# Kernel tuning notes

Measured on AMD Instinct MI355X. Metric: run time of the kernel, lower is better.

The kernel has to match this reference:

```python
import jax, jax.numpy as jnp
import numpy as np
from jax import lax

B, S, I, H, L = 128, 256, 64, 128, 64
N_SUB = 2  # fixed RK4 substeps per observation interval (replaces adaptive dopri5)


def setup_inputs() -> dict:
    key = jax.random.key(0)
    ks = jax.random.split(key, 16)
    sc = 0.05
    x = jax.random.normal(ks[0], (B, S, I), jnp.float32)
    # strictly increasing irregular observation times
    times = jnp.sort(jax.random.uniform(ks[1], (S,), jnp.float32) * 10.0)
    return {
        "x": x,
        "times": times,
        "W_ih": jax.random.normal(ks[2], (3 * H, I), jnp.float32) * sc,
        "W_hh": jax.random.normal(ks[3], (3 * H, H), jnp.float32) * sc,
        "b_ih": jnp.zeros((3 * H,), jnp.float32),
        "b_hh": jnp.zeros((3 * H,), jnp.float32),
        "ode_W1": jax.random.normal(ks[4], (H, H), jnp.float32) * sc,
        "ode_b1": jnp.zeros((H,), jnp.float32),
        "ode_W2": jax.random.normal(ks[5], (H, H), jnp.float32) * sc,
        "ode_b2": jnp.zeros((H,), jnp.float32),
        "W_mean": jax.random.normal(ks[6], (L, H), jnp.float32) * sc,
        "b_mean": jnp.zeros((L,), jnp.float32),
        "W_logvar": jax.random.normal(ks[7], (L, H), jnp.float32) * sc,
        "b_logvar": jnp.zeros((L,), jnp.float32),
    }


def reference(x, times, W_ih, W_hh, b_ih, b_hh, ode_W1, ode_b1, ode_W2, ode_b2,
              W_mean, b_mean, W_logvar, b_logvar):
    def ode_f(h):  # MLP dynamics: Linear -> tanh -> Linear (time-independent)
        return jnp.tanh(h @ ode_W1.T + ode_b1) @ ode_W2.T + ode_b2

    def rk4(h, dt):
        k1 = ode_f(h)
        k2 = ode_f(h + 0.5 * dt * k1)
        k3 = ode_f(h + 0.5 * dt * k2)
        k4 = ode_f(h + dt * k3)
        return h + (dt / 6.0) * (k1 + 2.0 * k2 + 2.0 * k3 + k4)

    def gru(x_t, h):  # torch.nn.GRUCell math
        gx = x_t @ W_ih.T + b_ih
        gh = h @ W_hh.T + b_hh
        rx, zx, nx = jnp.split(gx, 3, axis=-1)
        rh, zh, nh = jnp.split(gh, 3, axis=-1)
        r = jax.nn.sigmoid(rx + rh)
        z = jax.nn.sigmoid(zx + zh)
        n = jnp.tanh(nx + r * nh)
        return (1.0 - z) * n + z * h

    # iterate i = S-1 .. 0; before each GRU update (except the first, i=S-1)
    # evolve h from t_{i+1} backward to t_i  -> dt_i = t_i - t_{i+1} (negative)
    dt_rev = jnp.concatenate([jnp.zeros((1,), times.dtype),
                              (times[:-1] - times[1:])[::-1]])  # [S]
    x_rev = jnp.transpose(x[:, ::-1, :], (1, 0, 2))  # [S, B, I]

    def step(h, inp):
        x_t, dt = inp
        sub = dt / N_SUB
        for _ in range(N_SUB):  # fixed small unroll
            h = rk4(h, sub)
        h = gru(x_t, h)
        return h, None

    h0 = jnp.zeros((x.shape[0], W_hh.shape[1]), x.dtype)
    h, _ = lax.scan(step, h0, (x_rev, dt_rev))
    mean = h @ W_mean.T + b_mean
    logvar = h @ W_logvar.T + b_logvar
    return (mean, logvar)
```

## Files before the change

### kernel.cpp

```cpp
#include <hip/hip_runtime.h>

#define NB 128
#define NS 256
#define NI 64
#define NH 128
#define NL 64
#define NG 384

typedef _Float16 f16;
typedef __attribute__((ext_vector_type(2))) _Float16 f16x2;

__device__ __forceinline__ float fast_tanh(float x) {
    float e = __expf(2.0f * x);
    return 1.0f - 2.0f / (e + 1.0f);
}
__device__ __forceinline__ float fast_sig(float x) {
    return 1.0f / (1.0f + __expf(-x));
}
__device__ __forceinline__ float quad_red(float a) {
    a += __shfl_xor(a, 1);
    a += __shfl_xor(a, 2);
    return a;
}
__device__ __forceinline__ float fdot2(f16x2 a, f16x2 b, float c) {
#if __has_builtin(__builtin_amdgcn_fdot2)
    return __builtin_amdgcn_fdot2(a, b, c, false);
#else
    return c + (float)a.x * (float)b.x + (float)a.y * (float)b.y;
#endif
}
__device__ __forceinline__ f16x2 bc16(unsigned int u) {
    return __builtin_bit_cast(f16x2, u);
}

__device__ __align__(16) f16 g_W1h[NH * NH];
__device__ __align__(16) f16 g_W2h[NH * NH];
__device__ __align__(16) f16 g_W12h[NH * NH];
__device__ __align__(16) f16 g_Whhh[3 * NH * NH];
__device__ __align__(16) f16 g_Whh2h[3 * NH * NH];
__device__ float g_w1b2[NH];
__device__ float g_whhb2[3 * NH];

__global__ __launch_bounds__(384)
void gx_kernel(const float* __restrict__ x, const float* __restrict__ W_ih,
               const float* __restrict__ b_ih, float* __restrict__ gx)
{
    const int s = blockIdx.x;
    const int j = threadIdx.x;
    __shared__ __align__(16) float xs[NB * NI];
    for (int idx = j; idx < NB * NI; idx += 384) {
        int bb = idx >> 6, cc = idx & 63;
        xs[idx] = x[(bb * NS + s) * NI + cc];
    }
    float w[64];
#pragma unroll
    for (int c = 0; c < 64; c += 4)
        *(float4*)&w[c] = *(const float4*)&W_ih[j * NI + c];
    const float bj = b_ih[j];
    __syncthreads();
    for (int bb = 0; bb < NB; bb++) {
        const float* xr = xs + bb * NI;
        float a0 = 0.f, a1 = 0.f, a2 = 0.f, a3 = 0.f;
#pragma unroll
        for (int c = 0; c < 64; c += 4) {
            a0 = fmaf(w[c + 0], xr[c + 0], a0);
            a1 = fmaf(w[c + 1], xr[c + 1], a1);
            a2 = fmaf(w[c + 2], xr[c + 2], a2);
            a3 = fmaf(w[c + 3], xr[c + 3], a3);
        }
        gx[((size_t)s * NB + bb) * NG + j] = ((a0 + a1) + (a2 + a3)) + bj;
    }
}

__global__ __launch_bounds__(128)
void prep_kernel(const float* __restrict__ W1, const float* __restrict__ Whh,
                 const float* __restrict__ W2, const float* __restrict__ b2)
{
    const int i = blockIdx.x;
    const int j = threadIdx.x;
    __shared__ float rowA[NH];
    __shared__ float red[NH];
    const float* src = (i < NH) ? (W1 + i * NH) : (Whh + (size_t)(i - NH) * NH);
    rowA[j] = src[j];
    __syncthreads();
    float acc = 0.f;
    for (int k = 0; k < NH; k++) acc = fmaf(rowA[k], W2[k * NH + j], acc);
    if (i < NH) {
        g_W12h[i * NH + j] = (f16)acc;
        g_W1h[i * NH + j]  = (f16)rowA[j];
        g_W2h[i * NH + j]  = (f16)W2[i * NH + j];
    } else {
        g_Whh2h[(size_t)(i - NH) * NH + j] = (f16)acc;
        g_Whhh[(size_t)(i - NH) * NH + j]  = (f16)rowA[j];
    }
    red[j] = rowA[j] * b2[j];
    __syncthreads();
    for (int off = 64; off > 0; off >>= 1) {
        if (j < off) red[j] += red[j + off];
        __syncthreads();
    }
    if (j == 0) {
        if (i < NH) g_w1b2[i] = red[0];
        else        g_whhb2[i - NH] = red[0];
    }
}

#define CH(SRC, OBX) (*(const uint4*)((const unsigned char*)(SRC) + (OBX)))

#define DSTEP1(W, K, V, A0, A1)                                                \
    A0 = fdot2(W[K + 0], bc16((V).x), A0);                                     \
    A1 = fdot2(W[K + 1], bc16((V).y), A1);                                     \
    A0 = fdot2(W[K + 2], bc16((V).z), A0);                                     \
    A1 = fdot2(W[K + 3], bc16((V).w), A1);

#define DOT1(W, SRC, OUT)                                                      \
    {                                                                          \
        float a0_ = 0.f, a1_ = 0.f;                                            \
        { uint4 v_ = CH(SRC, ob0); DSTEP1(W, 0,  v_, a0_, a1_) }               \
        { uint4 v_ = CH(SRC, ob1); DSTEP1(W, 4,  v_, a0_, a1_) }               \
        { uint4 v_ = CH(SRC, ob2); DSTEP1(W, 8,  v_, a0_, a1_) }               \
        { uint4 v_ = CH(SRC, ob3); DSTEP1(W, 12, v_, a0_, a1_) }               \
        OUT = quad_red(a0_ + a1_);                                             \
    }

#define DOT2S(WA, WB, SRC, OA, OB)                                             \
    {                                                                          \
        float a0_ = 0.f, a1_ = 0.f, b0_ = 0.f, b1_ = 0.f;                      \
        { uint4 v_ = CH(SRC, ob0); DSTEP1(WA, 0,  v_, a0_, a1_) DSTEP1(WB, 0,  v_, b0_, b1_) } \
        { uint4 v_ = CH(SRC, ob1); DSTEP1(WA, 4,  v_, a0_, a1_) DSTEP1(WB, 4,  v_, b0_, b1_) } \
        { uint4 v_ = CH(SRC, ob2); DSTEP1(WA, 8,  v_, a0_, a1_) DSTEP1(WB, 8,  v_, b0_, b1_) } \
        { uint4 v_ = CH(SRC, ob3); DSTEP1(WA, 12, v_, a0_, a1_) DSTEP1(WB, 12, v_, b0_, b1_) } \
        OA = quad_red(a0_ + a1_);                                              \
        OB = quad_red(b0_ + b1_);                                              \
    }

#define DOT2D(WA, SA, WB, SB, OA, OB)                                          \
    {                                                                          \
        float a0_ = 0.f, a1_ = 0.f, b0_ = 0.f, b1_ = 0.f;                      \
        { uint4 v_ = CH(SA, ob0); uint4 u_ = CH(SB, ob0); DSTEP1(WA, 0,  v_, a0_, a1_) DSTEP1(WB, 0,  u_, b0_, b1_) } \
        { uint4 v_ = CH(SA, ob1); uint4 u_ = CH(SB, ob1); DSTEP1(WA, 4,  v_, a0_, a1_) DSTEP1(WB, 4,  u_, b0_, b1_) } \
        { uint4 v_ = CH(SA, ob2); uint4 u_ = CH(SB, ob2); DSTEP1(WA, 8,  v_, a0_, a1_) DSTEP1(WB, 8,  u_, b0_, b1_) } \
        { uint4 v_ = CH(SA, ob3); uint4 u_ = CH(SB, ob3); DSTEP1(WA, 12, v_, a0_, a1_) DSTEP1(WB, 12, u_, b0_, b1_) } \
        OA = quad_red(a0_ + a1_);                                              \
        OB = quad_red(b0_ + b1_);                                              \
    }

#define DOT4S(WA, WB, WC, WD, SRC, OA, OB, OC, OD)                             \
    {                                                                          \
        float a0_ = 0.f, a1_ = 0.f, b0_ = 0.f, b1_ = 0.f;                      \
        float c0_ = 0.f, c1_ = 0.f, d0_ = 0.f, d1_ = 0.f;                      \
        { uint4 v_ = CH(SRC, ob0); DSTEP1(WA, 0,  v_, a0_, a1_) DSTEP1(WB, 0,  v_, b0_, b1_) DSTEP1(WC, 0,  v_, c0_, c1_) DSTEP1(WD, 0,  v_, d0_, d1_) } \
        { uint4 v_ = CH(SRC, ob1); DSTEP1(WA, 4,  v_, a0_, a1_) DSTEP1(WB, 4,  v_, b0_, b1_) DSTEP1(WC, 4,  v_, c0_, c1_) DSTEP1(WD, 4,  v_, d0_, d1_) } \
        { uint4 v_ = CH(SRC, ob2); DSTEP1(WA, 8,  v_, a0_, a1_) DSTEP1(WB, 8,  v_, b0_, b1_) DSTEP1(WC, 8,  v_, c0_, c1_) DSTEP1(WD, 8,  v_, d0_, d1_) } \
        { uint4 v_ = CH(SRC, ob3); DSTEP1(WA, 12, v_, a0_, a1_) DSTEP1(WB, 12, v_, b0_, b1_) DSTEP1(WC, 12, v_, c0_, c1_) DSTEP1(WD, 12, v_, d0_, d1_) } \
        OA = quad_red(a0_ + a1_);                                              \
        OB = quad_red(b0_ + b1_);                                              \
        OC = quad_red(c0_ + c1_);                                              \
        OD = quad_red(d0_ + d1_);                                              \
    }

#define LOADW(DST, BASE)                                                       \
    {                                                                          \
        uint4 v0_ = *(const uint4*)((BASE) + cb0);                             \
        DST[0] = bc16(v0_.x); DST[1] = bc16(v0_.y); DST[2] = bc16(v0_.z); DST[3] = bc16(v0_.w); \
        uint4 v1_ = *(const uint4*)((BASE) + cb1);                             \
        DST[4] = bc16(v1_.x); DST[5] = bc16(v1_.y); DST[6] = bc16(v1_.z); DST[7] = bc16(v1_.w); \
        uint4 v2_ = *(const uint4*)((BASE) + cb2);                             \
        DST[8] = bc16(v2_.x); DST[9] = bc16(v2_.y); DST[10] = bc16(v2_.z); DST[11] = bc16(v2_.w); \
        uint4 v3_ = *(const uint4*)((BASE) + cb3);                             \
        DST[12] = bc16(v3_.x); DST[13] = bc16(v3_.y); DST[14] = bc16(v3_.z); DST[15] = bc16(v3_.w); \
    }

__global__ __launch_bounds__(512, 1)
void rnn_kernel(const float* __restrict__ times, const float* __restrict__ b_hh,
                const float* __restrict__ b1, const float* __restrict__ b2,
                const float* __restrict__ W_mean, const float* __restrict__ b_mean,
                const float* __restrict__ W_logvar, const float* __restrict__ b_logvar,
                const float* __restrict__ gx,
                const float* __restrict__ x, const float* __restrict__ W_ih,
                const float* __restrict__ b_ih,
                const int use_gx,
                float* __restrict__ out)
{
    const int b = blockIdx.x;
    const int t = threadIdx.x;
    const int r = t >> 2;
    const int p = t & 3;
    const int c0 = 32 * p;

    __shared__ __align__(16) f16 shHh[NH], shUh[NH], shAh[NH];
    __shared__ float shT[NS];
    __shared__ __align__(16) float shGX[NG], shX[NI], shHf[NH];

    const int cb0 = c0 + 8 * ((0 + p) & 3);
    const int cb1 = c0 + 8 * ((1 + p) & 3);
    const int cb2 = c0 + 8 * ((2 + p) & 3);
    const int cb3 = c0 + 8 * ((3 + p) & 3);
    const int ob0 = 2 * cb0, ob1 = 2 * cb1, ob2 = 2 * cb2, ob3 = 2 * cb3;

    f16x2 w1p[16], w2p[16], w12p[16];
    f16x2 wh0p[16], wh1p[16], wh2p[16];
    f16x2 ws0p[16], ws1p[16], ws2p[16];
    LOADW(w1p,  g_W1h  + r * NH);
    LOADW(w2p,  g_W2h  + r * NH);
    LOADW(w12p, g_W12h + r * NH);
    LOADW(wh0p, g_Whhh + (0 * NH + r) * NH);
    LOADW(wh1p, g_Whhh + (1 * NH + r) * NH);
    LOADW(wh2p, g_Whhh + (2 * NH + r) * NH);
    LOADW(ws0p, g_Whh2h + (size_t)(0 * NH + r) * NH);
    LOADW(ws1p, g_Whh2h + (size_t)(1 * NH + r) * NH);
    LOADW(ws2p, g_Whh2h + (size_t)(2 * NH + r) * NH);

    const float b1r = b1[r], b2r = b2[r];
    const float bh0 = b_hh[r], bh1 = b_hh[NH + r], bh2 = b_hh[2 * NH + r];
    const float w1b2r = g_w1b2[r];
    const float wb0 = g_whhb2[r], wb1 = g_whhb2[NH + r], wb2 = g_whhb2[2 * NH + r];

    if (t < NS) shT[t] = times[t];
    if (t < NH) shHh[t] = (f16)0.f;
    float h = 0.f;
    __syncthreads();

    for (int si = 0; si < NS; ++si) {
        const int seq = NS - 1 - si;
        const float dt = (si == 0) ? 0.f : (shT[seq] - shT[seq + 1]);
        const float dts = 0.5f * dt;
        const float a2 = 0.5f * dts;
        const float a6 = dts * (1.f / 6.f);

        float gxr = 0.f, gxz = 0.f, gxn = 0.f;
        if (use_gx) {
            const float* g = gx + ((size_t)seq * NB + b) * NG;
            gxr = g[r]; gxz = g[NH + r]; gxn = g[2 * NH + r];
        } else {
            if (t < NI) shX[t] = x[(b * NS + seq) * NI + t];
            __syncthreads();
            if (t < NG) {
                const float* wr = W_ih + t * NI;
                float a = 0.f;
#pragma unroll
                for (int cc = 0; cc < NI; cc += 4) {
                    float4 w4 = *(const float4*)(wr + cc);
                    a = fmaf(w4.x, shX[cc + 0], a);
                    a = fmaf(w4.y, shX[cc + 1], a);
                    a = fmaf(w4.z, shX[cc + 2], a);
                    a = fmaf(w4.w, shX[cc + 3], a);
                }
                shGX[t] = a + b_ih[t];
            }
            __syncthreads();
        }

        float z1a, u, S, m;
        DOT1(w1p, shHh, z1a);
        z1a += b1r;
        u = fast_tanh(z1a);
        S = u;
        if (p == 0) shUh[r] = (f16)u;
        __syncthreads();
        DOT1(w12p, shUh, m);
        u = fast_tanh(z1a + a2 * (m + w1b2r));
        S += 2.f * u;
        if (p == 0) shUh[r] = (f16)u;
        __syncthreads();
        DOT1(w12p, shUh, m);
        u = fast_tanh(z1a + a2 * (m + w1b2r));
        S += 2.f * u;
        if (p == 0) shUh[r] = (f16)u;
        __syncthreads();
        DOT1(w12p, shUh, m);
        u = fast_tanh(z1a + dts * (m + w1b2r));
        S += u;
        if (p == 0) shUh[r] = (f16)S;
        __syncthreads();
        float mA, mB;
        DOT2S(w2p, w12p, shUh, mA, mB);
        const float hA = h + a6 * mA + dts * b2r;
        const float z1b = z1a + a6 * mB + dts * w1b2r;
        u = fast_tanh(z1b);
        float S2 = u;
        if (p == 0) { shAh[r] = (f16)hA; shUh[r] = (f16)u; }
        __syncthreads();

        float g0, g1, g2;
        DOT2D(w12p, shUh, wh0p, shAh, m, g0);
        u = fast_tanh(z1b + a2 * (m + w1b2r));
        S2 += 2.f * u;
        if (p == 0) shUh[r] = (f16)u;
        __syncthreads();
        DOT2D(w12p, shUh, wh1p, shAh, m, g1);
        u = fast_tanh(z1b + a2 * (m + w1b2r));
        S2 += 2.f * u;
        if (p == 0) shUh[r] = (f16)u;
        __syncthreads();
        DOT2D(w12p, shUh, wh2p, shAh, m, g2);
        u = fast_tanh(z1b + dts * (m + w1b2r));
        S2 += u;
        if (p == 0) shUh[r] = (f16)S2;
        __syncthreads();
        float n0, n1, n2, n3;
        DOT4S(w2p, ws0p, ws1p, ws2p, shUh, n0, n1, n2, n3);
        const float hB = hA + a6 * n0 + dts * b2r;
        const float rh = g0 + a6 * n1 + dts * wb0 + bh0;
        const float zh = g1 + a6 * n2 + dts * wb1 + bh1;
        const float nh = g2 + a6 * n3 + dts * wb2 + bh2;
        float rx, zx, nx;
        if (use_gx) { rx = gxr; zx = gxz; nx = gxn; }
        else        { rx = shGX[r]; zx = shGX[NH + r]; nx = shGX[2 * NH + r]; }
        const float rr = fast_sig(rx + rh);
        const float zz = fast_sig(zx + zh);
        const float nn = fast_tanh(nx + rr * nh);
        h = (1.f - zz) * nn + zz * hB;
        if (p == 0) shHh[r] = (f16)h;
        __syncthreads();
    }

    if (p == 0) shHf[r] = h;
    __syncthreads();
    const int sel = r >> 6;
    const int l = r & 63;
    const float* Wf = sel ? W_logvar : W_mean;
    float a0 = 0.f, a1 = 0.f;
#pragma unroll
    for (int jj = 0; jj < 8; jj++) {
        float4 w4 = *(const float4*)&Wf[l * NH + c0 + 4 * jj];
        float4 h4 = *(const float4*)(shHf + c0 + 4 * jj);
        a0 = fmaf(w4.x, h4.x, a0);
        a1 = fmaf(w4.y, h4.y, a1);
        a0 = fmaf(w4.z, h4.z, a0);
        a1 = fmaf(w4.w, h4.w, a1);
    }
    float acc = quad_red(a0 + a1);
    if (p == 0) {
        const float bias = sel ? b_logvar[l] : b_mean[l];
        out[sel * (NB * NL) + b * NL + l] = acc + bias;
    }
}

extern "C" void kernel_launch(void* const* d_in, const int* in_sizes, int n_in,
                              void* d_out, int out_size, void* d_ws, size_t ws_size,
                              hipStream_t stream)
{
    const float* x        = (const float*)d_in[0];
    const float* times    = (const float*)d_in[1];
    const float* W_ih     = (const float*)d_in[2];
    const float* W_hh     = (const float*)d_in[3];
    const float* b_ih     = (const float*)d_in[4];
    const float* b_hh     = (const float*)d_in[5];
    const float* W1       = (const float*)d_in[6];
    const float* b1       = (const float*)d_in[7];
    const float* W2       = (const float*)d_in[8];
    const float* b2       = (const float*)d_in[9];
    const float* W_mean   = (const float*)d_in[10];
    const float* b_mean   = (const float*)d_in[11];
    const float* W_logvar = (const float*)d_in[12];
    const float* b_logvar = (const float*)d_in[13];
    float* out = (float*)d_out;

    float* gxbuf = (float*)d_ws;
    const size_t need = (size_t)NS * NB * NG * sizeof(float);
    const int use_gx = (d_ws != nullptr && ws_size >= need) ? 1 : 0;

    if (use_gx) {
        gx_kernel<<<NS, 384, 0, stream>>>(x, W_ih, b_ih, gxbuf);
    }
    prep_kernel<<<512, 128, 0, stream>>>(W1, W_hh, W2, b2);
    rnn_kernel<<<NB, 512, 0, stream>>>(times, b_hh, b1, b2,
                                       W_mean, b_mean, W_logvar, b_logvar,
                                       gxbuf, x, W_ih, b_ih, use_gx, out);
}
```

Baseline: 967.4 us.

## Halve threads per row to two lanes and prefetch next step's gx

The recurrent kernel now uses 256 threads per batch element, each hidden row split across 2 lanes of 64 columns instead of 4 lanes of 32. Each lane keeps twice as many fp16 weight registers and needs only one shuffle in its reduction instead of two. The input-gate values for the next timestep are loaded one iteration early so their global-memory latency overlaps the current step. In exchange, register pressure roughly doubles (9×32 packed weight registers per thread), and each lane's serial dot product is longer.

```diff
diff --git a/kernel.cpp b/kernel.cpp
--- a/kernel.cpp
+++ b/kernel.cpp
@@ -17,9 +17,8 @@
 __device__ __forceinline__ float fast_sig(float x) {
     return 1.0f / (1.0f + __expf(-x));
 }
-__device__ __forceinline__ float quad_red(float a) {
+__device__ __forceinline__ float red2(float a) {
     a += __shfl_xor(a, 1);
-    a += __shfl_xor(a, 2);
     return a;
 }
 __device__ __forceinline__ float fdot2(f16x2 a, f16x2 b, float c) {
@@ -105,9 +104,9 @@
     }
 }
 
-#define CH(SRC, OBX) (*(const uint4*)((const unsigned char*)(SRC) + (OBX)))
-
-#define DSTEP1(W, K, V, A0, A1)                                                \
+#define CHNK(SRC, OB) (*(const uint4*)((const unsigned char*)(SRC) + (OB)))
+
+#define D4(W, K, V, A0, A1)                                                    \
     A0 = fdot2(W[K + 0], bc16((V).x), A0);                                     \
     A1 = fdot2(W[K + 1], bc16((V).y), A1);                                     \
     A0 = fdot2(W[K + 2], bc16((V).z), A0);                                     \
@@ -116,62 +115,82 @@
 #define DOT1(W, SRC, OUT)                                                      \
     {                                                                          \
         float a0_ = 0.f, a1_ = 0.f;                                            \
-        { uint4 v_ = CH(SRC, ob0); DSTEP1(W, 0,  v_, a0_, a1_) }               \
-        { uint4 v_ = CH(SRC, ob1); DSTEP1(W, 4,  v_, a0_, a1_) }               \
-        { uint4 v_ = CH(SRC, ob2); DSTEP1(W, 8,  v_, a0_, a1_) }               \
-        { uint4 v_ = CH(SRC, ob3); DSTEP1(W, 12, v_, a0_, a1_) }               \
-        OUT = quad_red(a0_ + a1_);                                             \
+        { uint4 v_ = CHNK(SRC, ob0); D4(W, 0,  v_, a0_, a1_) }                 \
+        { uint4 v_ = CHNK(SRC, ob1); D4(W, 4,  v_, a0_, a1_) }                 \
+        { uint4 v_ = CHNK(SRC, ob2); D4(W, 8,  v_, a0_, a1_) }                 \
+        { uint4 v_ = CHNK(SRC, ob3); D4(W, 12, v_, a0_, a1_) }                 \
+        { uint4 v_ = CHNK(SRC, ob4); D4(W, 16, v_, a0_, a1_) }                 \
+        { uint4 v_ = CHNK(SRC, ob5); D4(W, 20, v_, a0_, a1_) }                 \
+        { uint4 v_ = CHNK(SRC, ob6); D4(W, 24, v_, a0_, a1_) }                 \
+        { uint4 v_ = CHNK(SRC, ob7); D4(W, 28, v_, a0_, a1_) }                 \
+        OUT = red2(a0_ + a1_);                                                 \
     }
 
 #define DOT2S(WA, WB, SRC, OA, OB)                                             \
     {                                                                          \
         float a0_ = 0.f, a1_ = 0.f, b0_ = 0.f, b1_ = 0.f;                      \
-        { uint4 v_ = CH(SRC, ob0); DSTEP1(WA, 0,  v_, a0_, a1_) DSTEP1(WB, 0,  v_, b0_, b1_) } \
-        { uint4 v_ = CH(SRC, ob1); DSTEP1(WA, 4,  v_, a0_, a1_) DSTEP1(WB, 4,  v_, b0_, b1_) } \
-        { uint4 v_ = CH(SRC, ob2); DSTEP1(WA, 8,  v_, a0_, a1_) DSTEP1(WB, 8,  v_, b0_, b1_) } \
-        { uint4 v_ = CH(SRC, ob3); DSTEP1(WA, 12, v_, a0_, a1_) DSTEP1(WB, 12, v_, b0_, b1_) } \
-        OA = quad_red(a0_ + a1_);                                              \
-        OB = quad_red(b0_ + b1_);                                              \
+        { uint4 v_ = CHNK(SRC, ob0); D4(WA, 0,  v_, a0_, a1_) D4(WB, 0,  v_, b0_, b1_) } \
+        { uint4 v_ = CHNK(SRC, ob1); D4(WA, 4,  v_, a0_, a1_) D4(WB, 4,  v_, b0_, b1_) } \
+        { uint4 v_ = CHNK(SRC, ob2); D4(WA, 8,  v_, a0_, a1_) D4(WB, 8,  v_, b0_, b1_) } \
+        { uint4 v_ = CHNK(SRC, ob3); D4(WA, 12, v_, a0_, a1_) D4(WB, 12, v_, b0_, b1_) } \
+        { uint4 v_ = CHNK(SRC, ob4); D4(WA, 16, v_, a0_, a1_) D4(WB, 16, v_, b0_, b1_) } \
+        { uint4 v_ = CHNK(SRC, ob5); D4(WA, 20, v_, a0_, a1_) D4(WB, 20, v_, b0_, b1_) } \
+        { uint4 v_ = CHNK(SRC, ob6); D4(WA, 24, v_, a0_, a1_) D4(WB, 24, v_, b0_, b1_) } \
+        { uint4 v_ = CHNK(SRC, ob7); D4(WA, 28, v_, a0_, a1_) D4(WB, 28, v_, b0_, b1_) } \
+        OA = red2(a0_ + a1_);                                                  \
+        OB = red2(b0_ + b1_);                                                  \
     }
 
 #define DOT2D(WA, SA, WB, SB, OA, OB)                                          \
     {                                                                          \
         float a0_ = 0.f, a1_ = 0.f, b0_ = 0.f, b1_ = 0.f;                      \
-        { uint4 v_ = CH(SA, ob0); uint4 u_ = CH(SB, ob0); DSTEP1(WA, 0,  v_, a0_, a1_) DSTEP1(WB, 0,  u_, b0_, b1_) } \
-        { uint4 v_ = CH(SA, ob1); uint4 u_ = CH(SB, ob1); DSTEP1(WA, 4,  v_, a0_, a1_) DSTEP1(WB, 4,  u_, b0_, b1_) } \
-        { uint4 v_ = CH(SA, ob2); uint4 u_ = CH(SB, ob2); DSTEP1(WA, 8,  v_, a0_, a1_) DSTEP1(WB, 8,  u_, b0_, b1_) } \
-        { uint4 v_ = CH(SA, ob3); uint4 u_ = CH(SB, ob3); DSTEP1(WA, 12, v_, a0_, a1_) DSTEP1(WB, 12, u_, b0_, b1_) } \
-        OA = quad_red(a0_ + a1_);                                              \
-        OB = quad_red(b0_ + b1_);                                              \
+        { uint4 v_ = CHNK(SA, ob0); uint4 u_ = CHNK(SB, ob0); D4(WA, 0,  v_, a0_, a1_) D4(WB, 0,  u_, b0_, b1_) } \
+        { uint4 v_ = CHNK(SA, ob1); uint4 u_ = CHNK(SB, ob1); D4(WA, 4,  v_, a0_, a1_) D4(WB, 4,  u_, b0_, b1_) } \
+        { uint4 v_ = CHNK(SA, ob2); uint4 u_ = CHNK(SB, ob2); D4(WA, 8,  v_, a0_, a1_) D4(WB, 8,  u_, b0_, b1_) } \
+        { uint4 v_ = CHNK(SA, ob3); uint4 u_ = CHNK(SB, ob3); D4(WA, 12, v_, a0_, a1_) D4(WB, 12, u_, b0_, b1_) } \
+        { uint4 v_ = CHNK(SA, ob4); uint4 u_ = CHNK(SB, ob4); D4(WA, 16, v_, a0_, a1_) D4(WB, 16, u_, b0_, b1_) } \
+        { uint4 v_ = CHNK(SA, ob5); uint4 u_ = CHNK(SB, ob5); D4(WA, 20, v_, a0_, a1_) D4(WB, 20, u_, b0_, b1_) } \
+        { uint4 v_ = CHNK(SA, ob6); uint4 u_ = CHNK(SB, ob6); D4(WA, 24, v_, a0_, a1_) D4(WB, 24, u_, b0_, b1_) } \
+        { uint4 v_ = CHNK(SA, ob7); uint4 u_ = CHNK(SB, ob7); D4(WA, 28, v_, a0_, a1_) D4(WB, 28, u_, b0_, b1_) } \
+        OA = red2(a0_ + a1_);                                                  \
+        OB = red2(b0_ + b1_);                                                  \
     }
 
 #define DOT4S(WA, WB, WC, WD, SRC, OA, OB, OC, OD)                             \
     {                                                                          \
         float a0_ = 0.f, a1_ = 0.f, b0_ = 0.f, b1_ = 0.f;                      \
         float c0_ = 0.f, c1_ = 0.f, d0_ = 0.f, d1_ = 0.f;                      \
-        { uint4 v_ = CH(SRC, ob0); DSTEP1(WA, 0,  v_, a0_, a1_) DSTEP1(WB, 0,  v_, b0_, b1_) DSTEP1(WC, 0,  v_, c0_, c1_) DSTEP1(WD, 0,  v_, d0_, d1_) } \
-        { uint4 v_ = CH(SRC, ob1); DSTEP1(WA, 4,  v_, a0_, a1_) DSTEP1(WB, 4,  v_, b0_, b1_) DSTEP1(WC, 4,  v_, c0_, c1_) DSTEP1(WD, 4,  v_, d0_, d1_) } \
-        { uint4 v_ = CH(SRC, ob2); DSTEP1(WA, 8,  v_, a0_, a1_) DSTEP1(WB, 8,  v_, b0_, b1_) DSTEP1(WC, 8,  v_, c0_, c1_) DSTEP1(WD, 8,  v_, d0_, d1_) } \
-        { uint4 v_ = CH(SRC, ob3); DSTEP1(WA, 12, v_, a0_, a1_) DSTEP1(WB, 12, v_, b0_, b1_) DSTEP1(WC, 12, v_, c0_, c1_) DSTEP1(WD, 12, v_, d0_, d1_) } \
-        OA = quad_red(a0_ + a1_);                                              \
-        OB = quad_red(b0_ + b1_);                                              \
-        OC = quad_red(c0_ + c1_);                                              \
-        OD = quad_red(d0_ + d1_);                                              \
+        { uint4 v_ = CHNK(SRC, ob0); D4(WA, 0,  v_, a0_, a1_) D4(WB, 0,  v_, b0_, b1_) D4(WC, 0,  v_, c0_, c1_) D4(WD, 0,  v_, d0_, d1_) } \
+        { uint4 v_ = CHNK(SRC, ob1); D4(WA, 4,  v_, a0_, a1_) D4(WB, 4,  v_, b0_, b1_) D4(WC, 4,  v_, c0_, c1_) D4(WD, 4,  v_, d0_, d1_) } \
+        { uint4 v_ = CHNK(SRC, ob2); D4(WA, 8,  v_, a0_, a1_) D4(WB, 8,  v_, b0_, b1_) D4(WC, 8,  v_, c0_, c1_) D4(WD, 8,  v_, d0_, d1_) } \
+        { uint4 v_ = CHNK(SRC, ob3); D4(WA, 12, v_, a0_, a1_) D4(WB, 12, v_, b0_, b1_) D4(WC, 12, v_, c0_, c1_) D4(WD, 12, v_, d0_, d1_) } \
+        { uint4 v_ = CHNK(SRC, ob4); D4(WA, 16, v_, a0_, a1_) D4(WB, 16, v_, b0_, b1_) D4(WC, 16, v_, c0_, c1_) D4(WD, 16, v_, d0_, d1_) } \
+        { uint4 v_ = CHNK(SRC, ob5); D4(WA, 20, v_, a0_, a1_) D4(WB, 20, v_, b0_, b1_) D4(WC, 20, v_, c0_, c1_) D4(WD, 20, v_, d0_, d1_) } \
+        { uint4 v_ = CHNK(SRC, ob6); D4(WA, 24, v_, a0_, a1_) D4(WB, 24, v_, b0_, b1_) D4(WC, 24, v_, c0_, c1_) D4(WD, 24, v_, d0_, d1_) } \
+        { uint4 v_ = CHNK(SRC, ob7); D4(WA, 28, v_, a0_, a1_) D4(WB, 28, v_, b0_, b1_) D4(WC, 28, v_, c0_, c1_) D4(WD, 28, v_, d0_, d1_) } \
+        OA = red2(a0_ + a1_);                                                  \
+        OB = red2(b0_ + b1_);                                                  \
+        OC = red2(c0_ + c1_);                                                  \
+        OD = red2(d0_ + d1_);                                                  \
+    }
+
+#define LDCH(DST, K, BP, OB)                                                   \
+    {                                                                          \
+        uint4 v_ = *(const uint4*)((BP) + (OB));                               \
+        DST[K + 0] = bc16(v_.x); DST[K + 1] = bc16(v_.y);                      \
+        DST[K + 2] = bc16(v_.z); DST[K + 3] = bc16(v_.w);                      \
     }
 
 #define LOADW(DST, BASE)                                                       \
     {                                                                          \
-        uint4 v0_ = *(const uint4*)((BASE) + cb0);                             \
-        DST[0] = bc16(v0_.x); DST[1] = bc16(v0_.y); DST[2] = bc16(v0_.z); DST[3] = bc16(v0_.w); \
-        uint4 v1_ = *(const uint4*)((BASE) + cb1);                             \
-        DST[4] = bc16(v1_.x); DST[5] = bc16(v1_.y); DST[6] = bc16(v1_.z); DST[7] = bc16(v1_.w); \
-        uint4 v2_ = *(const uint4*)((BASE) + cb2);                             \
-        DST[8] = bc16(v2_.x); DST[9] = bc16(v2_.y); DST[10] = bc16(v2_.z); DST[11] = bc16(v2_.w); \
-        uint4 v3_ = *(const uint4*)((BASE) + cb3);                             \
-        DST[12] = bc16(v3_.x); DST[13] = bc16(v3_.y); DST[14] = bc16(v3_.z); DST[15] = bc16(v3_.w); \
-    }
-
-__global__ __launch_bounds__(512, 1)
+        const unsigned char* bp_ = (const unsigned char*)(BASE);               \
+        LDCH(DST, 0,  bp_, ob0) LDCH(DST, 4,  bp_, ob1)                        \
+        LDCH(DST, 8,  bp_, ob2) LDCH(DST, 12, bp_, ob3)                        \
+        LDCH(DST, 16, bp_, ob4) LDCH(DST, 20, bp_, ob5)                        \
+        LDCH(DST, 24, bp_, ob6) LDCH(DST, 28, bp_, ob7)                        \
+    }
+
+__global__ __launch_bounds__(256, 1)
 void rnn_kernel(const float* __restrict__ times, const float* __restrict__ b_hh,
                 const float* __restrict__ b1, const float* __restrict__ b2,
                 const float* __restrict__ W_mean, const float* __restrict__ b_mean,
@@ -184,23 +203,25 @@
 {
     const int b = blockIdx.x;
     const int t = threadIdx.x;
-    const int r = t >> 2;
-    const int p = t & 3;
-    const int c0 = 32 * p;
+    const int r = t >> 1;
+    const int p = t & 1;
 
     __shared__ __align__(16) f16 shHh[NH], shUh[NH], shAh[NH];
     __shared__ float shT[NS];
     __shared__ __align__(16) float shGX[NG], shX[NI], shHf[NH];
 
-    const int cb0 = c0 + 8 * ((0 + p) & 3);
-    const int cb1 = c0 + 8 * ((1 + p) & 3);
-    const int cb2 = c0 + 8 * ((2 + p) & 3);
-    const int cb3 = c0 + 8 * ((3 + p) & 3);
-    const int ob0 = 2 * cb0, ob1 = 2 * cb1, ob2 = 2 * cb2, ob3 = 2 * cb3;
-
-    f16x2 w1p[16], w2p[16], w12p[16];
-    f16x2 wh0p[16], wh1p[16], wh2p[16];
-    f16x2 ws0p[16], ws1p[16], ws2p[16];
+    const int ob0 = 128 * p + 16 * ((0 + 4 * p) & 7);
+    const int ob1 = 128 * p + 16 * ((1 + 4 * p) & 7);
+    const int ob2 = 128 * p + 16 * ((2 + 4 * p) & 7);
+    const int ob3 = 128 * p + 16 * ((3 + 4 * p) & 7);
+    const int ob4 = 128 * p + 16 * ((4 + 4 * p) & 7);
+    const int ob5 = 128 * p + 16 * ((5 + 4 * p) & 7);
+    const int ob6 = 128 * p + 16 * ((6 + 4 * p) & 7);
+    const int ob7 = 128 * p + 16 * ((7 + 4 * p) & 7);
+
+    f16x2 w1p[32], w2p[32], w12p[32];
+    f16x2 wh0p[32], wh1p[32], wh2p[32];
+    f16x2 ws0p[32], ws1p[32], ws2p[32];
     LOADW(w1p,  g_W1h  + r * NH);
     LOADW(w2p,  g_W2h  + r * NH);
     LOADW(w12p, g_W12h + r * NH);
@@ -221,6 +242,12 @@
     float h = 0.f;
     __syncthreads();
 
+    float gxr = 0.f, gxz = 0.f, gxn = 0.f;
+    if (use_gx) {
+        const float* g = gx + ((size_t)(NS - 1) * NB + b) * NG;
+        gxr = g[r]; gxz = g[NH + r]; gxn = g[2 * NH + r];
+    }
+
     for (int si = 0; si < NS; ++si) {
         const int seq = NS - 1 - si;
         const float dt = (si == 0) ? 0.f : (shT[seq] - shT[seq + 1]);
@@ -228,15 +255,16 @@
         const float a2 = 0.5f * dts;
         const float a6 = dts * (1.f / 6.f);
 
-        float gxr = 0.f, gxz = 0.f, gxn = 0.f;
+        float gnr = 0.f, gnz = 0.f, gnn = 0.f;
         if (use_gx) {
-            const float* g = gx + ((size_t)seq * NB + b) * NG;
-            gxr = g[r]; gxz = g[NH + r]; gxn = g[2 * NH + r];
+            const int seqn = (seq > 0) ? (seq - 1) : 0;
+            const float* g = gx + ((size_t)seqn * NB + b) * NG;
+            gnr = g[r]; gnz = g[NH + r]; gnn = g[2 * NH + r];
         } else {
             if (t < NI) shX[t] = x[(b * NS + seq) * NI + t];
             __syncthreads();
-            if (t < NG) {
-                const float* wr = W_ih + t * NI;
+            for (int idx = t; idx < NG; idx += 256) {
+                const float* wr = W_ih + idx * NI;
                 float a = 0.f;
 #pragma unroll
                 for (int cc = 0; cc < NI; cc += 4) {
@@ -246,7 +274,7 @@
                     a = fmaf(w4.z, shX[cc + 2], a);
                     a = fmaf(w4.w, shX[cc + 3], a);
                 }
-                shGX[t] = a + b_ih[t];
+                shGX[idx] = a + b_ih[idx];
             }
             __syncthreads();
         }
@@ -312,6 +340,7 @@
         const float nn = fast_tanh(nx + rr * nh);
         h = (1.f - zz) * nn + zz * hB;
         if (p == 0) shHh[r] = (f16)h;
+        gxr = gnr; gxz = gnz; gxn = gnn;
         __syncthreads();
     }
 
@@ -320,17 +349,18 @@
     const int sel = r >> 6;
     const int l = r & 63;
     const float* Wf = sel ? W_logvar : W_mean;
+    const int hc0 = 64 * p;
     float a0 = 0.f, a1 = 0.f;
 #pragma unroll
-    for (int jj = 0; jj < 8; jj++) {
-        float4 w4 = *(const float4*)&Wf[l * NH + c0 + 4 * jj];
-        float4 h4 = *(const float4*)(shHf + c0 + 4 * jj);
+    for (int jj = 0; jj < 16; jj++) {
+        float4 w4 = *(const float4*)&Wf[l * NH + hc0 + 4 * jj];
+        float4 h4 = *(const float4*)(shHf + hc0 + 4 * jj);
         a0 = fmaf(w4.x, h4.x, a0);
         a1 = fmaf(w4.y, h4.y, a1);
         a0 = fmaf(w4.z, h4.z, a0);
         a1 = fmaf(w4.w, h4.w, a1);
     }
-    float acc = quad_red(a0 + a1);
+    float acc = red2(a0 + a1);
     if (p == 0) {
         const float bias = sel ? b_logvar[l] : b_mean[l];
         out[sel * (NB * NL) + b * NL + l] = acc + bias;
@@ -365,7 +395,7 @@
         gx_kernel<<<NS, 384, 0, stream>>>(x, W_ih, b_ih, gxbuf);
     }
     prep_kernel<<<512, 128, 0, stream>>>(W1, W_hh, W2, b2);
-    rnn_kernel<<<NB, 512, 0, stream>>>(times, b_hh, b1, b2,
+    rnn_kernel<<<NB, 256, 0, stream>>>(times, b_hh, b1, b2,
                                        W_mean, b_mean, W_logvar, b_logvar,
                                        gxbuf, x, W_ih, b_ih, use_gx, out);
 }
```

After: 1.061 ms. 9.7% more time.

## Use DPP quad reductions, lighter LDS barriers, and prefetch next-step gate inputs

Applied to the files above, without the earlier changes.

Replaces the shfl_xor quad reductions with DPP row-permute adds and the full __syncthreads with an LDS-only waitcnt plus s_barrier, to cut latency on the serial recurrence's critical path. It also prefetches the next timestep's precomputed input-gate values one iteration ahead, adds more independent dot-product accumulators in the small dot macros for ILP, and changes the launch bounds to allow two blocks per CU. The risks are register pressure from launch_bounds(512,2) causing weight-register spills, and subtle ordering hazards from the custom barrier.

```diff
diff --git a/kernel.cpp b/kernel.cpp
--- a/kernel.cpp
+++ b/kernel.cpp
@@ -17,9 +17,15 @@
 __device__ __forceinline__ float fast_sig(float x) {
     return 1.0f / (1.0f + __expf(-x));
 }
+template <int CTRL>
+__device__ __forceinline__ float dpp_xor_add(float a) {
+    int ai = __builtin_bit_cast(int, a);
+    int bi = __builtin_amdgcn_update_dpp(0, ai, CTRL, 0xF, 0xF, true);
+    return a + __builtin_bit_cast(float, bi);
+}
 __device__ __forceinline__ float quad_red(float a) {
-    a += __shfl_xor(a, 1);
-    a += __shfl_xor(a, 2);
+    a = dpp_xor_add<0xB1>(a);
+    a = dpp_xor_add<0x4E>(a);
     return a;
 }
 __device__ __forceinline__ float fdot2(f16x2 a, f16x2 b, float c) {
@@ -31,6 +37,11 @@
 }
 __device__ __forceinline__ f16x2 bc16(unsigned int u) {
     return __builtin_bit_cast(f16x2, u);
+}
+__device__ __forceinline__ void sync_lds() {
+    asm volatile("s_waitcnt lgkmcnt(0)" ::: "memory");
+    __builtin_amdgcn_s_barrier();
+    asm volatile("" ::: "memory");
 }
 
 __device__ __align__(16) f16 g_W1h[NH * NH];
@@ -105,9 +116,15 @@
     }
 }
 
-#define CH(SRC, OBX) (*(const uint4*)((const unsigned char*)(SRC) + (OBX)))
-
-#define DSTEP1(W, K, V, A0, A1)                                                \
+#define CHNK(SRC, OB) (*(const uint4*)((const unsigned char*)(SRC) + (OB)))
+
+#define D4(W, K, V, A0, A1, A2, A3)                                            \
+    A0 = fdot2(W[K + 0], bc16((V).x), A0);                                     \
+    A1 = fdot2(W[K + 1], bc16((V).y), A1);                                     \
+    A2 = fdot2(W[K + 2], bc16((V).z), A2);                                     \
+    A3 = fdot2(W[K + 3], bc16((V).w), A3);
+
+#define D2(W, K, V, A0, A1)                                                    \
     A0 = fdot2(W[K + 0], bc16((V).x), A0);                                     \
     A1 = fdot2(W[K + 1], bc16((V).y), A1);                                     \
     A0 = fdot2(W[K + 2], bc16((V).z), A0);                                     \
@@ -115,63 +132,67 @@
 
 #define DOT1(W, SRC, OUT)                                                      \
     {                                                                          \
-        float a0_ = 0.f, a1_ = 0.f;                                            \
-        { uint4 v_ = CH(SRC, ob0); DSTEP1(W, 0,  v_, a0_, a1_) }               \
-        { uint4 v_ = CH(SRC, ob1); DSTEP1(W, 4,  v_, a0_, a1_) }               \
-        { uint4 v_ = CH(SRC, ob2); DSTEP1(W, 8,  v_, a0_, a1_) }               \
-        { uint4 v_ = CH(SRC, ob3); DSTEP1(W, 12, v_, a0_, a1_) }               \
-        OUT = quad_red(a0_ + a1_);                                             \
+        float a0_ = 0.f, a1_ = 0.f, a2_ = 0.f, a3_ = 0.f;                      \
+        { uint4 v_ = CHNK(SRC, ob0); D4(W, 0,  v_, a0_, a1_, a2_, a3_) }       \
+        { uint4 v_ = CHNK(SRC, ob1); D4(W, 4,  v_, a0_, a1_, a2_, a3_) }       \
+        { uint4 v_ = CHNK(SRC, ob2); D4(W, 8,  v_, a0_, a1_, a2_, a3_) }       \
+        { uint4 v_ = CHNK(SRC, ob3); D4(W, 12, v_, a0_, a1_, a2_, a3_) }       \
+        OUT = quad_red((a0_ + a1_) + (a2_ + a3_));                             \
     }
 
 #define DOT2S(WA, WB, SRC, OA, OB)                                             \
     {                                                                          \
-        float a0_ = 0.f, a1_ = 0.f, b0_ = 0.f, b1_ = 0.f;                      \
-        { uint4 v_ = CH(SRC, ob0); DSTEP1(WA, 0,  v_, a0_, a1_) DSTEP1(WB, 0,  v_, b0_, b1_) } \
-        { uint4 v_ = CH(SRC, ob1); DSTEP1(WA, 4,  v_, a0_, a1_) DSTEP1(WB, 4,  v_, b0_, b1_) } \
-        { uint4 v_ = CH(SRC, ob2); DSTEP1(WA, 8,  v_, a0_, a1_) DSTEP1(WB, 8,  v_, b0_, b1_) } \
-        { uint4 v_ = CH(SRC, ob3); DSTEP1(WA, 12, v_, a0_, a1_) DSTEP1(WB, 12, v_, b0_, b1_) } \
-        OA = quad_red(a0_ + a1_);                                              \
-        OB = quad_red(b0_ + b1_);                                              \
+        float a0_ = 0.f, a1_ = 0.f, a2_ = 0.f, a3_ = 0.f;                      \
+        float b0_ = 0.f, b1_ = 0.f, b2_ = 0.f, b3_ = 0.f;                      \
+        { uint4 v_ = CHNK(SRC, ob0); D4(WA, 0,  v_, a0_, a1_, a2_, a3_) D4(WB, 0,  v_, b0_, b1_, b2_, b3_) } \
+        { uint4 v_ = CHNK(SRC, ob1); D4(WA, 4,  v_, a0_, a1_, a2_, a3_) D4(WB, 4,  v_, b0_, b1_, b2_, b3_) } \
+        { uint4 v_ = CHNK(SRC, ob2); D4(WA, 8,  v_, a0_, a1_, a2_, a3_) D4(WB, 8,  v_, b0_, b1_, b2_, b3_) } \
+        { uint4 v_ = CHNK(SRC, ob3); D4(WA, 12, v_, a0_, a1_, a2_, a3_) D4(WB, 12, v_, b0_, b1_, b2_, b3_) } \
+        OA = quad_red((a0_ + a1_) + (a2_ + a3_));                              \
+        OB = quad_red((b0_ + b1_) + (b2_ + b3_));                              \
     }
 
 #define DOT2D(WA, SA, WB, SB, OA, OB)                                          \
     {                                                                          \
-        float a0_ = 0.f, a1_ = 0.f, b0_ = 0.f, b1_ = 0.f;                      \
-        { uint4 v_ = CH(SA, ob0); uint4 u_ = CH(SB, ob0); DSTEP1(WA, 0,  v_, a0_, a1_) DSTEP1(WB, 0,  u_, b0_, b1_) } \
-        { uint4 v_ = CH(SA, ob1); uint4 u_ = CH(SB, ob1); DSTEP1(WA, 4,  v_, a0_, a1_) DSTEP1(WB, 4,  u_, b0_, b1_) } \
-        { uint4 v_ = CH(SA, ob2); uint4 u_ = CH(SB, ob2); DSTEP1(WA, 8,  v_, a0_, a1_) DSTEP1(WB, 8,  u_, b0_, b1_) } \
-        { uint4 v_ = CH(SA, ob3); uint4 u_ = CH(SB, ob3); DSTEP1(WA, 12, v_, a0_, a1_) DSTEP1(WB, 12, u_, b0_, b1_) } \
-        OA = quad_red(a0_ + a1_);                                              \
-        OB = quad_red(b0_ + b1_);                                              \
+        float a0_ = 0.f, a1_ = 0.f, a2_ = 0.f, a3_ = 0.f;                      \
+        float b0_ = 0.f, b1_ = 0.f, b2_ = 0.f, b3_ = 0.f;                      \
+        { uint4 v_ = CHNK(SA, ob0); uint4 u_ = CHNK(SB, ob0); D4(WA, 0,  v_, a0_, a1_, a2_, a3_) D4(WB, 0,  u_, b0_, b1_, b2_, b3_) } \
+        { uint4 v_ = CHNK(SA, ob1); uint4 u_ = CHNK(SB, ob1); D4(WA, 4,  v_, a0_, a1_, a2_, a3_) D4(WB, 4,  u_, b0_, b1_, b2_, b3_) } \
+        { uint4 v_ = CHNK(SA, ob2); uint4 u_ = CHNK(SB, ob2); D4(WA, 8,  v_, a0_, a1_, a2_, a3_) D4(WB, 8,  u_, b0_, b1_, b2_, b3_) } \
+        { uint4 v_ = CHNK(SA, ob3); uint4 u_ = CHNK(SB, ob3); D4(WA, 12, v_, a0_, a1_, a2_, a3_) D4(WB, 12, u_, b0_, b1_, b2_, b3_) } \
+        OA = quad_red((a0_ + a1_) + (a2_ + a3_));                              \
+        OB = quad_red((b0_ + b1_) + (b2_ + b3_));                              \
     }
 
 #define DOT4S(WA, WB, WC, WD, SRC, OA, OB, OC, OD)                             \
     {                                                                          \
         float a0_ = 0.f, a1_ = 0.f, b0_ = 0.f, b1_ = 0.f;                      \
         float c0_ = 0.f, c1_ = 0.f, d0_ = 0.f, d1_ = 0.f;                      \
-        { uint4 v_ = CH(SRC, ob0); DSTEP1(WA, 0,  v_, a0_, a1_) DSTEP1(WB, 0,  v_, b0_, b1_) DSTEP1(WC, 0,  v_, c0_, c1_) DSTEP1(WD, 0,  v_, d0_, d1_) } \
-        { uint4 v_ = CH(SRC, ob1); DSTEP1(WA, 4,  v_, a0_, a1_) DSTEP1(WB, 4,  v_, b0_, b1_) DSTEP1(WC, 4,  v_, c0_, c1_) DSTEP1(WD, 4,  v_, d0_, d1_) } \
-        { uint4 v_ = CH(SRC, ob2); DSTEP1(WA, 8,  v_, a0_, a1_) DSTEP1(WB, 8,  v_, b0_, b1_) DSTEP1(WC, 8,  v_, c0_, c1_) DSTEP1(WD, 8,  v_, d0_, d1_) } \
-        { uint4 v_ = CH(SRC, ob3); DSTEP1(WA, 12, v_, a0_, a1_) DSTEP1(WB, 12, v_, b0_, b1_) DSTEP1(WC, 12, v_, c0_, c1_) DSTEP1(WD, 12, v_, d0_, d1_) } \
+        { uint4 v_ = CHNK(SRC, ob0); D2(WA, 0,  v_, a0_, a1_) D2(WB, 0,  v_, b0_, b1_) D2(WC, 0,  v_, c0_, c1_) D2(WD, 0,  v_, d0_, d1_) } \
+        { uint4 v_ = CHNK(SRC, ob1); D2(WA, 4,  v_, a0_, a1_) D2(WB, 4,  v_, b0_, b1_) D2(WC, 4,  v_, c0_, c1_) D2(WD, 4,  v_, d0_, d1_) } \
+        { uint4 v_ = CHNK(SRC, ob2); D2(WA, 8,  v_, a0_, a1_) D2(WB, 8,  v_, b0_, b1_) D2(WC, 8,  v_, c0_, c1_) D2(WD, 8,  v_, d0_, d1_) } \
+        { uint4 v_ = CHNK(SRC, ob3); D2(WA, 12, v_, a0_, a1_) D2(WB, 12, v_, b0_, b1_) D2(WC, 12, v_, c0_, c1_) D2(WD, 12, v_, d0_, d1_) } \
         OA = quad_red(a0_ + a1_);                                              \
         OB = quad_red(b0_ + b1_);                                              \
         OC = quad_red(c0_ + c1_);                                              \
         OD = quad_red(d0_ + d1_);                                              \
     }
 
+#define LDCH(DST, K, BP, OB)                                                   \
+    {                                                                          \
+        uint4 v_ = *(const uint4*)((BP) + (OB));                               \
+        DST[K + 0] = bc16(v_.x); DST[K + 1] = bc16(v_.y);                      \
+        DST[K + 2] = bc16(v_.z); DST[K + 3] = bc16(v_.w);                      \
+    }
+
 #define LOADW(DST, BASE)                                                       \
     {                                                                          \
-        uint4 v0_ = *(const uint4*)((BASE) + cb0);                             \
-        DST[0] = bc16(v0_.x); DST[1] = bc16(v0_.y); DST[2] = bc16(v0_.z); DST[3] = bc16(v0_.w); \
-        uint4 v1_ = *(const uint4*)((BASE) + cb1);                             \
-        DST[4] = bc16(v1_.x); DST[5] = bc16(v1_.y); DST[6] = bc16(v1_.z); DST[7] = bc16(v1_.w); \
-        uint4 v2_ = *(const uint4*)((BASE) + cb2);                             \
-        DST[8] = bc16(v2_.x); DST[9] = bc16(v2_.y); DST[10] = bc16(v2_.z); DST[11] = bc16(v2_.w); \
-        uint4 v3_ = *(const uint4*)((BASE) + cb3);                             \
-        DST[12] = bc16(v3_.x); DST[13] = bc16(v3_.y); DST[14] = bc16(v3_.z); DST[15] = bc16(v3_.w); \
-    }
-
-__global__ __launch_bounds__(512, 1)
+        const unsigned char* bp_ = (const unsigned char*)(BASE);               \
+        LDCH(DST, 0, bp_, ob0) LDCH(DST, 4, bp_, ob1)                          \
+        LDCH(DST, 8, bp_, ob2) LDCH(DST, 12, bp_, ob3)                         \
+    }
+
+__global__ __launch_bounds__(512, 2)
 void rnn_kernel(const float* __restrict__ times, const float* __restrict__ b_hh,
                 const float* __restrict__ b1, const float* __restrict__ b2,
                 const float* __restrict__ W_mean, const float* __restrict__ b_mean,
@@ -186,17 +207,15 @@
     const int t = threadIdx.x;
     const int r = t >> 2;
     const int p = t & 3;
-    const int c0 = 32 * p;
 
     __shared__ __align__(16) f16 shHh[NH], shUh[NH], shAh[NH];
     __shared__ float shT[NS];
     __shared__ __align__(16) float shGX[NG], shX[NI], shHf[NH];
 
-    const int cb0 = c0 + 8 * ((0 + p) & 3);
-    const int cb1 = c0 + 8 * ((1 + p) & 3);
-    const int cb2 = c0 + 8 * ((2 + p) & 3);
-    const int cb3 = c0 + 8 * ((3 + p) & 3);
-    const int ob0 = 2 * cb0, ob1 = 2 * cb1, ob2 = 2 * cb2, ob3 = 2 * cb3;
+    const int ob0 = 64 * p + 16 * ((0 + p) & 3);
+    const int ob1 = 64 * p + 16 * ((1 + p) & 3);
+    const int ob2 = 64 * p + 16 * ((2 + p) & 3);
+    const int ob3 = 64 * p + 16 * ((3 + p) & 3);
 
     f16x2 w1p[16], w2p[16], w12p[16];
     f16x2 wh0p[16], wh1p[16], wh2p[16];
@@ -221,6 +240,12 @@
     float h = 0.f;
     __syncthreads();
 
+    float gxr = 0.f, gxz = 0.f, gxn = 0.f;
+    if (use_gx) {
+        const float* g = gx + ((size_t)(NS - 1) * NB + b) * NG;
+        gxr = g[r]; gxz = g[NH + r]; gxn = g[2 * NH + r];
+    }
+
     for (int si = 0; si < NS; ++si) {
         const int seq = NS - 1 - si;
         const float dt = (si == 0) ? 0.f : (shT[seq] - shT[seq + 1]);
@@ -228,10 +253,11 @@
         const float a2 = 0.5f * dts;
         const float a6 = dts * (1.f / 6.f);
 
-        float gxr = 0.f, gxz = 0.f, gxn = 0.f;
+        float gnr = 0.f, gnz = 0.f, gnn = 0.f;
         if (use_gx) {
-            const float* g = gx + ((size_t)seq * NB + b) * NG;
-            gxr = g[r]; gxz = g[NH + r]; gxn = g[2 * NH + r];
+            const int seqn = (seq > 0) ? (seq - 1) : 0;
+            const float* g = gx + ((size_t)seqn * NB + b) * NG;
+            gnr = g[r]; gnz = g[NH + r]; gnn = g[2 * NH + r];
         } else {
             if (t < NI) shX[t] = x[(b * NS + seq) * NI + t];
             __syncthreads();
@@ -257,22 +283,22 @@
         u = fast_tanh(z1a);
         S = u;
         if (p == 0) shUh[r] = (f16)u;
-        __syncthreads();
+        sync_lds();
         DOT1(w12p, shUh, m);
         u = fast_tanh(z1a + a2 * (m + w1b2r));
         S += 2.f * u;
         if (p == 0) shUh[r] = (f16)u;
-        __syncthreads();
+        sync_lds();
         DOT1(w12p, shUh, m);
         u = fast_tanh(z1a + a2 * (m + w1b2r));
         S += 2.f * u;
         if (p == 0) shUh[r] = (f16)u;
-        __syncthreads();
+        sync_lds();
         DOT1(w12p, shUh, m);
         u = fast_tanh(z1a + dts * (m + w1b2r));
         S += u;
         if (p == 0) shUh[r] = (f16)S;
-        __syncthreads();
+        sync_lds();
         float mA, mB;
         DOT2S(w2p, w12p, shUh, mA, mB);
         const float hA = h + a6 * mA + dts * b2r;
@@ -280,24 +306,24 @@
         u = fast_tanh(z1b);
         float S2 = u;
         if (p == 0) { shAh[r] = (f16)hA; shUh[r] = (f16)u; }
-        __syncthreads();
+        sync_lds();
 
         float g0, g1, g2;
         DOT2D(w12p, shUh, wh0p, shAh, m, g0);
         u = fast_tanh(z1b + a2 * (m + w1b2r));
         S2 += 2.f * u;
         if (p == 0) shUh[r] = (f16)u;
-        __syncthreads();
+        sync_lds();
         DOT2D(w12p, shUh, wh1p, shAh, m, g1);
         u = fast_tanh(z1b + a2 * (m + w1b2r));
         S2 += 2.f * u;
         if (p == 0) shUh[r] = (f16)u;
-        __syncthreads();
+        sync_lds();
         DOT2D(w12p, shUh, wh2p, shAh, m, g2);
         u = fast_tanh(z1b + dts * (m + w1b2r));
         S2 += u;
         if (p == 0) shUh[r] = (f16)S2;
-        __syncthreads();
+        sync_lds();
         float n0, n1, n2, n3;
         DOT4S(w2p, ws0p, ws1p, ws2p, shUh, n0, n1, n2, n3);
         const float hB = hA + a6 * n0 + dts * b2r;
@@ -312,7 +338,8 @@
         const float nn = fast_tanh(nx + rr * nh);
         h = (1.f - zz) * nn + zz * hB;
         if (p == 0) shHh[r] = (f16)h;
-        __syncthreads();
+        gxr = gnr; gxz = gnz; gxn = gnn;
+        sync_lds();
     }
 
     if (p == 0) shHf[r] = h;
@@ -320,6 +347,7 @@
     const int sel = r >> 6;
     const int l = r & 63;
     const float* Wf = sel ? W_logvar : W_mean;
+    const int c0 = 32 * p;
     float a0 = 0.f, a1 = 0.f;
 #pragma unroll
     for (int jj = 0; jj < 8; jj++) {
```

Measured after the change: 912.1 us, median of 2. 1.06x faster.
